# Kernel tuning notes

Hardware: AMD Instinct MI355X
Metric: run time of the kernel (lower is better)

Reference implementation:

```python
import jax, jax.numpy as jnp
import numpy as np

B, S, D_MODEL, H, D = 2, 2048, 1024, 16, 64
SCALE = 1.0 / float(np.sqrt(D))


def setup_inputs() -> dict:
    key = jax.random.key(0)
    ks = jax.random.split(key, 5)
    x = jax.random.normal(ks[0], (B, S, D_MODEL), jnp.float32)
    qkv_w = jax.random.normal(ks[1], (3 * H * D, D_MODEL), jnp.float32) * 0.02
    out_w = jax.random.normal(ks[2], (D_MODEL, H * D), jnp.float32) * 0.02
    bias_p = jax.random.uniform(ks[3], (H, 1, 1), jnp.float32) * 2.0  # torch.rand(...)*2
    bias_a = jax.random.uniform(ks[4], (H, 1, 1), jnp.float32)
    # standard geometric RoPE frequencies over d_head//2 = 32 channels
    rope_freqs = 10000.0 ** (-jnp.arange(D // 2, dtype=jnp.float32) / (D // 2))
    return {"x": x, "qkv_w": qkv_w, "out_w": out_w,
            "bias_p": bias_p, "bias_a": bias_a, "rope_freqs": rope_freqs}


def _rope(t, c, s):
    # t: [B,H,S,d]; c,s: [1,1,S,d/2]. Split-half rotation as in apply_rope.
    d2 = t.shape[-1] // 2
    t1, t2 = t[..., :d2], t[..., d2:]
    return jnp.concatenate([t1 * c - t2 * s, t1 * s + t2 * c], axis=-1)


def reference(x, qkv_w, out_w, bias_p, bias_a, rope_freqs):
    Bb, Ss, _ = x.shape
    qkv = (x @ qkv_w.T).reshape(Bb, Ss, 3, H, D)
    q = qkv[:, :, 0].transpose(0, 2, 1, 3)  # [B,H,S,d]
    k = qkv[:, :, 1].transpose(0, 2, 1, 3)
    v = qkv[:, :, 2].transpose(0, 2, 1, 3)
    pos = jnp.arange(Ss, dtype=jnp.float32)
    ang = pos[:, None] * rope_freqs[None, :]                 # [S, d/2]
    c = jnp.cos(ang)[None, None]
    s = jnp.sin(ang)[None, None]
    q = _rope(q, c, s)
    k = _rope(k, c, s)
    scores = jnp.einsum('bhqd,bhkd->bhqk', q, k) * SCALE     # [B,H,S,S]
    p = jnp.maximum(bias_p, 0.01)                            # clamp(min=0.01)
    a = jnp.maximum(bias_a, 0.01)
    dist = jnp.abs(pos[None, :] - pos[:, None])              # [S,S]
    kb = -p * jnp.log1p(a * dist)                            # [H,S,S]
    attn = jax.nn.softmax(scores + kb[None], axis=-1)
    out = jnp.einsum('bhqk,bhkd->bhqd', attn, v)             # [B,H,S,d]
    out = out.transpose(0, 2, 1, 3).reshape(Bb, Ss, H * D)
    return out @ out_w.T
```

## Files before the change

### kernel.cpp

```cpp
#include <hip/hip_runtime.h>
#include <math.h>

#define BATCH  2
#define SEQ    2048
#define DMODEL 1024
#define NH     16
#define HD     64
#define NQKV   3072
#define ROWS   (BATCH*SEQ)
#define QSCALE 0.18033688f

typedef unsigned short u16;
typedef unsigned int   u32;
typedef __bf16 bf16x8 __attribute__((ext_vector_type(8)));
typedef float  f32x4  __attribute__((ext_vector_type(4)));

typedef const __attribute__((address_space(1))) void* gptr_t;
typedef __attribute__((address_space(3))) void* lptr_t;

__device__ __forceinline__ void gload16(lptr_t l, const void* g) {
    __builtin_amdgcn_global_load_lds((gptr_t)g, l, 16, 0, 0);
}

__device__ __forceinline__ u16 f2bf(float f) {
    unsigned int u = __float_as_uint(f);
    u += 0x7FFFu + ((u >> 16) & 1u);
    return (u16)(u >> 16);
}
__device__ __forceinline__ u32 pk2(float lo, float hi) {
#if __has_builtin(__builtin_amdgcn_cvt_pk_bf16_f32)
    typedef __bf16 bf16x2 __attribute__((ext_vector_type(2)));
    union { bf16x2 v; u32 u; } cv;
    cv.v = __builtin_amdgcn_cvt_pk_bf16_f32(lo, hi);
    return cv.u;
#else
    return (u32)f2bf(lo) | ((u32)f2bf(hi) << 16);
#endif
}
__device__ __forceinline__ float fexp2(float x) {
#if __has_builtin(__builtin_amdgcn_exp2f)
    return __builtin_amdgcn_exp2f(x);
#else
    return exp2f(x);
#endif
}

#define NBC ((ROWS*DMODEL + NQKV*DMODEL + DMODEL*DMODEL) / 1024)
__global__ void prep_kernel(const float* __restrict__ a,
                            const float* __restrict__ b,
                            const float* __restrict__ c,
                            u16* __restrict__ oa, u16* __restrict__ ob,
                            u16* __restrict__ oc,
                            const float* __restrict__ freqs, float* __restrict__ cs_tab,
                            const float* __restrict__ bias_p,
                            const float* __restrict__ bias_a,
                            float* __restrict__ wtab)
{
    const int na = ROWS*DMODEL, nb = NQKV*DMODEL;
    int blk = blockIdx.x;
    if (blk < NBC) {
        int i = (blk * 256 + threadIdx.x) * 4;
        const float* s; u16* d; int base;
        if (i < na)           { s = a; d = oa; base = i; }
        else if (i < na + nb) { s = b; d = ob; base = i - na; }
        else                  { s = c; d = oc; base = i - na - nb; }
        float4 v = *(const float4*)(s + base);
        u16 o[4] = { f2bf(v.x), f2bf(v.y), f2bf(v.z), f2bf(v.w) };
        *(uint2*)(d + base) = *(const uint2*)o;
    } else if (blk < NBC + 256) {
        int idx = (blk - NBC) * 256 + threadIdx.x;
        int s = idx >> 5, d = idx & 31;
        float sn, cs;
        sincosf((float)s * freqs[d], &sn, &cs);
        cs_tab[idx * 2]     = cs;
        cs_tab[idx * 2 + 1] = sn;
    } else {
        int idx = (blk - NBC - 256) * 256 + threadIdx.x;
        int h = idx >> 11;
        int d = idx & (SEQ - 1);
        float p = fmaxf(bias_p[h], 0.01f);
        float aa = fmaxf(bias_a[h], 0.01f);
        wtab[idx] = __expf(-p * log1pf(aa * (float)d));
    }
}

__global__ __launch_bounds__(256) void gemm_qkv(
    const u16* __restrict__ A, const u16* __restrict__ B,
    const float* __restrict__ cs_tab,
    u16* __restrict__ Qb, u16* __restrict__ Kb, u16* __restrict__ Vt)
{
    const int K = DMODEL;
    __shared__ __align__(16) u16 As[128][32];
    __shared__ __align__(16) u16 Bs[128][32];
    const int tid  = threadIdx.x;
    const int wave = tid >> 6, lane = tid & 63;
    const int quad = lane >> 4, l16 = lane & 15;
    const int wrow = (wave >> 1) * 64, wcol = (wave & 1) * 64;
    const int bm = blockIdx.x * 128, bn = blockIdx.y * 128;

    const int srow = lane >> 2;
    const int scol = ((lane & 3) ^ (srow & 3)) * 8;
    const int fsw = (quad ^ (l16 & 3)) * 8;

    f32x4 acc[4][4];
#pragma unroll
    for (int i = 0; i < 4; ++i)
#pragma unroll
        for (int j = 0; j < 4; ++j) acc[i][j] = (f32x4){0.f,0.f,0.f,0.f};

    const u16* Ag0 = A + (size_t)(bm + wave*32 + srow)      * K + scol;
    const u16* Ag1 = A + (size_t)(bm + wave*32 + 16 + srow) * K + scol;
    const u16* Bg0 = B + (size_t)(bn + wave*32 + srow)      * K + scol;
    const u16* Bg1 = B + (size_t)(bn + wave*32 + 16 + srow) * K + scol;

    for (int k0 = 0; k0 < K; k0 += 32) {
        __syncthreads();
        gload16((lptr_t)&As[wave*32][0],      Ag0 + k0);
        gload16((lptr_t)&As[wave*32 + 16][0], Ag1 + k0);
        gload16((lptr_t)&Bs[wave*32][0],      Bg0 + k0);
        gload16((lptr_t)&Bs[wave*32 + 16][0], Bg1 + k0);
        __syncthreads();
        bf16x8 af[4], bfr[4];
#pragma unroll
        for (int i = 0; i < 4; ++i)
            af[i] = *(const bf16x8*)&As[wrow + i*16 + l16][fsw];
#pragma unroll
        for (int j = 0; j < 4; ++j)
            bfr[j] = *(const bf16x8*)&Bs[wcol + j*16 + l16][fsw];
#pragma unroll
        for (int i = 0; i < 4; ++i)
#pragma unroll
            for (int j = 0; j < 4; ++j)
                acc[i][j] = __builtin_amdgcn_mfma_f32_16x16x32_bf16(af[i], bfr[j], acc[i][j], 0, 0, 0);
    }

    const int tcol = (bn + wcol) >> 6;
    const int t = tcol >> 4, h = tcol & 15;
    const int bq = bm >> 11;
    const int sb = (bm & (SEQ - 1)) + wrow;
    const size_t hb = (size_t)(bq * NH + h) * SEQ * HD;

    if (t == 2) {
#pragma unroll
        for (int i = 0; i < 4; ++i) {
            const int s = sb + i*16 + quad*4;
#pragma unroll
            for (int j = 0; j < 4; ++j) {
                const int d = j*16 + l16;
                uint2 pv = make_uint2(pk2(acc[i][j][0], acc[i][j][1]),
                                      pk2(acc[i][j][2], acc[i][j][3]));
                *(uint2*)&Vt[hb + (size_t)d * SEQ + s] = pv;
            }
        }
    } else {
        const float sc = (t == 0) ? QSCALE : 1.0f;
        u16* dstb = ((t == 0) ? Qb : Kb) + hb;
#pragma unroll
        for (int i = 0; i < 4; ++i) {
#pragma unroll
            for (int r = 0; r < 4; ++r) {
                const int s = sb + i*16 + quad*4 + r;
                const float2* ct = (const float2*)(cs_tab + ((size_t)s * 32 + l16) * 2);
                float2 cs0 = ct[0];
                float2 cs1 = ct[16];
                float a0 = acc[i][0][r], a1 = acc[i][1][r];
                float a2 = acc[i][2][r], a3 = acc[i][3][r];
                u16* dst = dstb + (size_t)s * HD;
                dst[l16]      = f2bf((a0*cs0.x - a2*cs0.y) * sc);
                dst[16 + l16] = f2bf((a1*cs1.x - a3*cs1.y) * sc);
                dst[32 + l16] = f2bf((a0*cs0.y + a2*cs0.x) * sc);
                dst[48 + l16] = f2bf((a1*cs1.y + a3*cs1.x) * sc);
            }
        }
    }
}

__global__ __launch_bounds__(256) void gemm_out(
    const u16* __restrict__ A, const u16* __restrict__ B,
    float* __restrict__ Cout, int M, int N, int K)
{
    __shared__ __align__(16) u16 As[128][32];
    __shared__ __align__(16) u16 Bs[64][32];
    const int tid  = threadIdx.x;
    const int wave = tid >> 6, lane = tid & 63;
    const int quad = lane >> 4, l16 = lane & 15;
    const int wrow = (wave >> 1) * 64, wcol = (wave & 1) * 32;
    const int bm = blockIdx.x * 128, bn = blockIdx.y * 64;

    const int srow = lane >> 2;
    const int scol = ((lane & 3) ^ (srow & 3)) * 8;
    const int fsw = (quad ^ (l16 & 3)) * 8;

    f32x4 acc[4][2];
#pragma unroll
    for (int i = 0; i < 4; ++i)
#pragma unroll
        for (int j = 0; j < 2; ++j) acc[i][j] = (f32x4){0.f,0.f,0.f,0.f};

    const u16* Ag0 = A + (size_t)(bm + wave*32 + srow)      * K + scol;
    const u16* Ag1 = A + (size_t)(bm + wave*32 + 16 + srow) * K + scol;
    const u16* Bg0 = B + (size_t)(bn + wave*16 + srow)      * K + scol;

    for (int k0 = 0; k0 < K; k0 += 32) {
        __syncthreads();
        gload16((lptr_t)&As[wave*32][0],      Ag0 + k0);
        gload16((lptr_t)&As[wave*32 + 16][0], Ag1 + k0);
        gload16((lptr_t)&Bs[wave*16][0],      Bg0 + k0);
        __syncthreads();
        bf16x8 af[4], bfr[2];
#pragma unroll
        for (int i = 0; i < 4; ++i)
            af[i] = *(const bf16x8*)&As[wrow + i*16 + l16][fsw];
#pragma unroll
        for (int j = 0; j < 2; ++j)
            bfr[j] = *(const bf16x8*)&Bs[wcol + j*16 + l16][fsw];
#pragma unroll
        for (int i = 0; i < 4; ++i)
#pragma unroll
            for (int j = 0; j < 2; ++j)
                acc[i][j] = __builtin_amdgcn_mfma_f32_16x16x32_bf16(af[i], bfr[j], acc[i][j], 0, 0, 0);
    }

#pragma unroll
    for (int i = 0; i < 4; ++i)
#pragma unroll
        for (int j = 0; j < 2; ++j) {
            int col = bn + wcol + j*16 + l16;
#pragma unroll
            for (int r = 0; r < 4; ++r) {
                int row = bm + wrow + i*16 + quad*4 + r;
                Cout[(size_t)row * N + col] = acc[i][j][r];
            }
        }
}

__global__ __launch_bounds__(256, 3) void attn_mfma(
    const u16* __restrict__ Qb, const u16* __restrict__ Kb,
    const u16* __restrict__ Vt, const float* __restrict__ wtab,
    u16* __restrict__ attn_bf)
{
    __shared__ __align__(16) u16 Vs[2][64*128];
    __shared__ __align__(16) u16 Ps[4*64*32];
    __shared__ u32 ws2[2][192];
    __shared__ float lred[4][64];
    __shared__ float linv[64];

    const int tid = threadIdx.x;
    const int wave = tid >> 6, lane = tid & 63;
    const int quad = lane >> 4, l16 = lane & 15;
    const int q0 = blockIdx.x * 64, h = blockIdx.y, b = blockIdx.z;

    const u16* Qh = Qb + (size_t)(b * NH + h) * SEQ * HD;
    const u16* Kh = Kb + (size_t)(b * NH + h) * SEQ * HD;
    const u16* Vh = Vt + (size_t)(b * NH + h) * HD * SEQ;
    const float* wh = wtab + h * SEQ;

    bf16x8 qf0[4], qf1[4];
#pragma unroll
    for (int qj = 0; qj < 4; ++qj) {
        const u16* qr = Qh + (size_t)(q0 + qj*16 + l16) * HD + quad * 8;
        qf0[qj] = *(const bf16x8*)qr;
        qf1[qj] = *(const bf16x8*)(qr + 32);
    }

    const u16* Kf0 = Kh + (size_t)(wave*32 + l16) * HD + quad * 8;

    const int vsrow = lane >> 4;
    const u16* Vst[4];
#pragma unroll
    for (int i = 0; i < 4; ++i) {
        int d = wave*16 + i*4 + vsrow;
        int vscol = ((lane & 15) ^ (d & 7)) * 8;
        Vst[i] = Vh + (size_t)d * SEQ + vscol;
    }

    const int psw  = ((l16 >> 1) & 3) << 3;
    const int mb0  = 127 + l16 - wave*32 - quad*4 - 3;

    float l_p[4] = {0.f, 0.f, 0.f, 0.f};
    f32x4 o[4];
#pragma unroll
    for (int j = 0; j < 4; ++j) o[j] = (f32x4){0.f,0.f,0.f,0.f};

#pragma unroll
    for (int i = 0; i < 4; ++i)
        gload16((lptr_t)&Vs[0][(wave*16 + i*4)*128], Vst[i]);
    if (tid < 192) {
        int i0 = (q0 - 127) + tid;
        int a0 = i0 < 0 ? -i0 : i0;  if (a0 > SEQ-1) a0 = SEQ-1;
        int i1 = i0 + 1;
        int a1 = i1 < 0 ? -i1 : i1;  if (a1 > SEQ-1) a1 = SEQ-1;
        ws2[0][tid] = pk2(wh[a0], wh[a1]);
    }
    __syncthreads();

    for (int kt = 0; kt < SEQ / 128; ++kt) {
        const int k0 = kt * 128;
        const int cur = kt & 1;
        const u32* wsb = ws2[cur];

        bf16x8 kf[2][2];
#pragma unroll
        for (int kg = 0; kg < 2; ++kg) {
            const u16* kp = Kf0 + (size_t)(k0 + kg*16) * HD;
            kf[kg][0] = *(const bf16x8*)kp;
            kf[kg][1] = *(const bf16x8*)(kp + 32);
        }

        if (kt + 1 < SEQ / 128) {
#pragma unroll
            for (int i = 0; i < 4; ++i)
                gload16((lptr_t)&Vs[cur ^ 1][(wave*16 + i*4)*128],
                        Vst[i] + k0 + 128);
        }

#pragma unroll
        for (int kg = 0; kg < 2; ++kg) {
#pragma unroll
            for (int qj = 0; qj < 4; ++qj) {
                f32x4 zz = (f32x4){0.f,0.f,0.f,0.f};
                zz = __builtin_amdgcn_mfma_f32_16x16x32_bf16(kf[kg][0], qf0[qj], zz, 0, 0, 0);
                zz = __builtin_amdgcn_mfma_f32_16x16x32_bf16(kf[kg][1], qf1[qj], zz, 0, 0, 0);
                const int mbase = mb0 + qj*16 - kg*16;
                u32 pA = wsb[mbase], pB = wsb[mbase + 2];
                float w3 = __uint_as_float(pA << 16);
                float w2 = __uint_as_float(pA & 0xffff0000u);
                float w1 = __uint_as_float(pB << 16);
                float w0 = __uint_as_float(pB & 0xffff0000u);
                float e0 = fexp2(zz[0]) * w0, e1 = fexp2(zz[1]) * w1;
                float e2 = fexp2(zz[2]) * w2, e3 = fexp2(zz[3]) * w3;
                l_p[qj] += (e0 + e1) + (e2 + e3);
                *(uint2*)&Ps[wave*2048 + (qj*16 + l16)*32
                             + ((kg*16 + quad*4) ^ psw)] =
                    make_uint2(pk2(e0, e1), pk2(e2, e3));
            }
        }
        __syncthreads();

        bf16x8 pf[4];
#pragma unroll
        for (int m = 0; m < 4; ++m)
            pf[m] = *(const bf16x8*)&Ps[m*2048 + (wave*16 + l16)*32
                                        + ((quad*8) ^ psw)];
#pragma unroll
        for (int j = 0; j < 4; ++j) {
            const int vrow = (j*16 + l16) * 128;
            const int vsw = l16 & 7;
#pragma unroll
            for (int m = 0; m < 4; ++m) {
                bf16x8 vf = *(const bf16x8*)&Vs[cur][vrow + (((m*4 + quad) ^ vsw) * 8)];
                o[j] = __builtin_amdgcn_mfma_f32_16x16x32_bf16(pf[m], vf, o[j], 0, 0, 0);
            }
        }

        if (kt + 1 < SEQ / 128 && tid < 192) {
            int i0 = (q0 - (k0 + 128) - 127) + tid;
            int a0 = i0 < 0 ? -i0 : i0;  if (a0 > SEQ-1) a0 = SEQ-1;
            int i1 = i0 + 1;
            int a1 = i1 < 0 ? -i1 : i1;  if (a1 > SEQ-1) a1 = SEQ-1;
            ws2[cur ^ 1][tid] = pk2(wh[a0], wh[a1]);
        }
        __syncthreads();
    }

#pragma unroll
    for (int qj = 0; qj < 4; ++qj) {
        float l = l_p[qj];
        l += __shfl_xor(l, 16);
        l += __shfl_xor(l, 32);
        if (quad == 0) lred[wave][qj*16 + l16] = l;
    }
    __syncthreads();
    if (tid < 64)
        linv[tid] = 1.0f / (lred[0][tid] + lred[1][tid] + lred[2][tid] + lred[3][tid]);
    __syncthreads();
#pragma unroll
    for (int r = 0; r < 4; ++r) {
        const int q = wave*16 + quad*4 + r;
        float inv = linv[q];
        u16* dst = attn_bf + (size_t)(b * SEQ + q0 + q) * DMODEL + h * HD;
#pragma unroll
        for (int j = 0; j < 4; ++j)
            dst[j*16 + l16] = f2bf(o[j][r] * inv);
    }
}

extern "C" void kernel_launch(void* const* d_in, const int* in_sizes, int n_in,
                              void* d_out, int out_size, void* d_ws, size_t ws_size,
                              hipStream_t stream)
{
    (void)in_sizes; (void)n_in; (void)out_size; (void)ws_size;
    const float* x      = (const float*)d_in[0];
    const float* qkv_w  = (const float*)d_in[1];
    const float* out_w  = (const float*)d_in[2];
    const float* bias_p = (const float*)d_in[3];
    const float* bias_a = (const float*)d_in[4];
    const float* freqs  = (const float*)d_in[5];
    float* out = (float*)d_out;

    char* ws = (char*)d_ws;
    u16*   attn_bf = (u16*)ws;
    u16*   Qb      = (u16*)(ws + 8388608);
    u16*   x_bf    = (u16*)(ws + 25165824);
    u16*   w1_bf   = (u16*)(ws + 33554432);
    u16*   w2_bf   = (u16*)(ws + 39845888);
    u16*   Kb      = (u16*)(ws + 41943040);
    u16*   Vt      = (u16*)(ws + 50331648);
    float* wtab    = (float*)(ws + 58720256);
    float* cs_tab  = (float*)(ws + 58720256 + 131072);

    prep_kernel<<<dim3(NBC + 256 + 128), 256, 0, stream>>>(
        x, qkv_w, out_w, x_bf, w1_bf, w2_bf, freqs, cs_tab, bias_p, bias_a, wtab);

    gemm_qkv<<<dim3(ROWS/128, NQKV/128), 256, 0, stream>>>(x_bf, w1_bf, cs_tab, Qb, Kb, Vt);
    attn_mfma<<<dim3(SEQ/64, NH, BATCH), 256, 0, stream>>>(Qb, Kb, Vt, wtab, attn_bf);
    gemm_out<<<dim3(ROWS/128, DMODEL/64), 256, 0, stream>>>(attn_bf, w2_bf, out, ROWS, DMODEL, DMODEL);
}
```

Measured before the change: 239.4 us.

## Keep P in registers by giving each wave its own query rows

The attention kernel changes its work split. Each wave now owns 16 query rows and computes scores against all 128 keys of a tile, instead of owning a slice of keys across all 64 queries. The exponentiated probabilities stay in registers and feed the PV MFMA directly, which removes the Ps shared-memory round trip, a per-tile __syncthreads, and the cross-wave row-sum reduction. V fragments are now assembled from two 8-byte LDS reads to match the register layout of P, K loads are split into two halves around a sched_barrier, and launch bounds rise to 4 blocks per CU; each wave now reads every K row of a tile itself, so per-block K traffic grows.

```diff
diff --git a/kernel.cpp b/kernel.cpp
--- a/kernel.cpp
+++ b/kernel.cpp
@@ -8,6 +8,7 @@
 #define HD     64
 #define NQKV   3072
 #define ROWS   (BATCH*SEQ)
+#define NT     (SEQ/128)
 #define QSCALE 0.18033688f
 
 typedef unsigned short u16;
@@ -234,15 +235,13 @@
         }
 }
 
-__global__ __launch_bounds__(256, 3) void attn_mfma(
+__global__ __launch_bounds__(256, 4) void attn_mfma(
     const u16* __restrict__ Qb, const u16* __restrict__ Kb,
     const u16* __restrict__ Vt, const float* __restrict__ wtab,
     u16* __restrict__ attn_bf)
 {
     __shared__ __align__(16) u16 Vs[2][64*128];
-    __shared__ __align__(16) u16 Ps[4*64*32];
     __shared__ u32 ws2[2][192];
-    __shared__ float lred[4][64];
     __shared__ float linv[64];
 
     const int tid = threadIdx.x;
@@ -255,15 +254,11 @@
     const u16* Vh = Vt + (size_t)(b * NH + h) * HD * SEQ;
     const float* wh = wtab + h * SEQ;
 
-    bf16x8 qf0[4], qf1[4];
-#pragma unroll
-    for (int qj = 0; qj < 4; ++qj) {
-        const u16* qr = Qh + (size_t)(q0 + qj*16 + l16) * HD + quad * 8;
-        qf0[qj] = *(const bf16x8*)qr;
-        qf1[qj] = *(const bf16x8*)(qr + 32);
-    }
-
-    const u16* Kf0 = Kh + (size_t)(wave*32 + l16) * HD + quad * 8;
+    const u16* qr = Qh + (size_t)(q0 + wave*16 + l16) * HD + quad * 8;
+    const bf16x8 qf0 = *(const bf16x8*)qr;
+    const bf16x8 qf1 = *(const bf16x8*)(qr + 32);
+
+    const u16* Kf = Kh + (size_t)l16 * HD + quad * 8;
 
     const int vsrow = lane >> 4;
     const u16* Vst[4];
@@ -274,10 +269,9 @@
         Vst[i] = Vh + (size_t)d * SEQ + vscol;
     }
 
-    const int psw  = ((l16 >> 1) & 3) << 3;
-    const int mb0  = 127 + l16 - wave*32 - quad*4 - 3;
-
-    float l_p[4] = {0.f, 0.f, 0.f, 0.f};
+    const int mb0 = 127 + wave*16 + l16 - quad*4 - 3;
+
+    float l_p = 0.f;
     f32x4 o[4];
 #pragma unroll
     for (int j = 0; j < 4; ++j) o[j] = (f32x4){0.f,0.f,0.f,0.f};
@@ -294,67 +288,91 @@
     }
     __syncthreads();
 
-    for (int kt = 0; kt < SEQ / 128; ++kt) {
-        const int k0 = kt * 128;
+    for (int kt = 0; kt < NT; ++kt) {
         const int cur = kt & 1;
         const u32* wsb = ws2[cur];
-
-        bf16x8 kf[2][2];
-#pragma unroll
-        for (int kg = 0; kg < 2; ++kg) {
-            const u16* kp = Kf0 + (size_t)(k0 + kg*16) * HD;
-            kf[kg][0] = *(const bf16x8*)kp;
-            kf[kg][1] = *(const bf16x8*)(kp + 32);
-        }
-
-        if (kt + 1 < SEQ / 128) {
+        const u16* Kt = Kf + (size_t)(kt * 128) * HD;
+        u32 y[16];
+        bf16x8 ka[8];
+
+#pragma unroll
+        for (int g = 0; g < 4; ++g) {
+            const u16* kp = Kt + (size_t)(g * 16) * HD;
+            ka[2*g]   = *(const bf16x8*)kp;
+            ka[2*g+1] = *(const bf16x8*)(kp + 32);
+        }
+#pragma unroll
+        for (int g = 0; g < 4; ++g) {
+            f32x4 z = (f32x4){0.f,0.f,0.f,0.f};
+            z = __builtin_amdgcn_mfma_f32_16x16x32_bf16(ka[2*g],   qf0, z, 0, 0, 0);
+            z = __builtin_amdgcn_mfma_f32_16x16x32_bf16(ka[2*g+1], qf1, z, 0, 0, 0);
+            const int mbase = mb0 - 16*g;
+            u32 pA = wsb[mbase], pB = wsb[mbase + 2];
+            float w3 = __uint_as_float(pA << 16);
+            float w2 = __uint_as_float(pA & 0xffff0000u);
+            float w1 = __uint_as_float(pB << 16);
+            float w0 = __uint_as_float(pB & 0xffff0000u);
+            float e0 = fexp2(z[0]) * w0, e1 = fexp2(z[1]) * w1;
+            float e2 = fexp2(z[2]) * w2, e3 = fexp2(z[3]) * w3;
+            l_p += (e0 + e1) + (e2 + e3);
+            y[2*g]   = pk2(e0, e1);
+            y[2*g+1] = pk2(e2, e3);
+        }
+
+#pragma unroll
+        for (int g = 0; g < 4; ++g) {
+            const u16* kp = Kt + (size_t)((g + 4) * 16) * HD;
+            ka[2*g]   = *(const bf16x8*)kp;
+            ka[2*g+1] = *(const bf16x8*)(kp + 32);
+        }
+        __builtin_amdgcn_sched_barrier(0);
+
+        if (kt + 1 < NT) {
 #pragma unroll
             for (int i = 0; i < 4; ++i)
                 gload16((lptr_t)&Vs[cur ^ 1][(wave*16 + i*4)*128],
-                        Vst[i] + k0 + 128);
-        }
-
-#pragma unroll
-        for (int kg = 0; kg < 2; ++kg) {
-#pragma unroll
-            for (int qj = 0; qj < 4; ++qj) {
-                f32x4 zz = (f32x4){0.f,0.f,0.f,0.f};
-                zz = __builtin_amdgcn_mfma_f32_16x16x32_bf16(kf[kg][0], qf0[qj], zz, 0, 0, 0);
-                zz = __builtin_amdgcn_mfma_f32_16x16x32_bf16(kf[kg][1], qf1[qj], zz, 0, 0, 0);
-                const int mbase = mb0 + qj*16 - kg*16;
-                u32 pA = wsb[mbase], pB = wsb[mbase + 2];
-                float w3 = __uint_as_float(pA << 16);
-                float w2 = __uint_as_float(pA & 0xffff0000u);
-                float w1 = __uint_as_float(pB << 16);
-                float w0 = __uint_as_float(pB & 0xffff0000u);
-                float e0 = fexp2(zz[0]) * w0, e1 = fexp2(zz[1]) * w1;
-                float e2 = fexp2(zz[2]) * w2, e3 = fexp2(zz[3]) * w3;
-                l_p[qj] += (e0 + e1) + (e2 + e3);
-                *(uint2*)&Ps[wave*2048 + (qj*16 + l16)*32
-                             + ((kg*16 + quad*4) ^ psw)] =
-                    make_uint2(pk2(e0, e1), pk2(e2, e3));
+                        Vst[i] + (kt + 1) * 128);
+        }
+
+#pragma unroll
+        for (int g = 0; g < 4; ++g) {
+            f32x4 z = (f32x4){0.f,0.f,0.f,0.f};
+            z = __builtin_amdgcn_mfma_f32_16x16x32_bf16(ka[2*g],   qf0, z, 0, 0, 0);
+            z = __builtin_amdgcn_mfma_f32_16x16x32_bf16(ka[2*g+1], qf1, z, 0, 0, 0);
+            const int mbase = mb0 - 16*(g + 4);
+            u32 pA = wsb[mbase], pB = wsb[mbase + 2];
+            float w3 = __uint_as_float(pA << 16);
+            float w2 = __uint_as_float(pA & 0xffff0000u);
+            float w1 = __uint_as_float(pB << 16);
+            float w0 = __uint_as_float(pB & 0xffff0000u);
+            float e0 = fexp2(z[0]) * w0, e1 = fexp2(z[1]) * w1;
+            float e2 = fexp2(z[2]) * w2, e3 = fexp2(z[3]) * w3;
+            l_p += (e0 + e1) + (e2 + e3);
+            y[8 + 2*g] = pk2(e0, e1);
+            y[9 + 2*g] = pk2(e2, e3);
+        }
+
+#pragma unroll
+        for (int s = 0; s < 4; ++s) {
+            union { u32 u[4]; bf16x8 v; } pfu;
+            pfu.u[0] = y[4*s];     pfu.u[1] = y[4*s + 1];
+            pfu.u[2] = y[4*s + 2]; pfu.u[3] = y[4*s + 3];
+#pragma unroll
+            for (int j = 0; j < 4; ++j) {
+                const int d = j*16 + l16;
+                const int rb = d*128 + (quad & 1)*4;
+                const int c0 = (4*s     + (quad >> 1)) ^ (l16 & 7);
+                const int c1 = (4*s + 2 + (quad >> 1)) ^ (l16 & 7);
+                uint2 va = *(const uint2*)&Vs[cur][rb + c0*8];
+                uint2 vb = *(const uint2*)&Vs[cur][rb + c1*8];
+                union { uint4 u; bf16x8 v; } vfu;
+                vfu.u = make_uint4(va.x, va.y, vb.x, vb.y);
+                o[j] = __builtin_amdgcn_mfma_f32_16x16x32_bf16(pfu.v, vfu.v, o[j], 0, 0, 0);
             }
         }
-        __syncthreads();
-
-        bf16x8 pf[4];
-#pragma unroll
-        for (int m = 0; m < 4; ++m)
-            pf[m] = *(const bf16x8*)&Ps[m*2048 + (wave*16 + l16)*32
-                                        + ((quad*8) ^ psw)];
-#pragma unroll
-        for (int j = 0; j < 4; ++j) {
-            const int vrow = (j*16 + l16) * 128;
-            const int vsw = l16 & 7;
-#pragma unroll
-            for (int m = 0; m < 4; ++m) {
-                bf16x8 vf = *(const bf16x8*)&Vs[cur][vrow + (((m*4 + quad) ^ vsw) * 8)];
-                o[j] = __builtin_amdgcn_mfma_f32_16x16x32_bf16(pf[m], vf, o[j], 0, 0, 0);
-            }
-        }
-
-        if (kt + 1 < SEQ / 128 && tid < 192) {
-            int i0 = (q0 - (k0 + 128) - 127) + tid;
+
+        if (kt + 1 < NT && tid < 192) {
+            int i0 = (q0 - (kt + 1)*128 - 127) + tid;
             int a0 = i0 < 0 ? -i0 : i0;  if (a0 > SEQ-1) a0 = SEQ-1;
             int i1 = i0 + 1;
             int a1 = i1 < 0 ? -i1 : i1;  if (a1 > SEQ-1) a1 = SEQ-1;
@@ -363,16 +381,9 @@
         __syncthreads();
     }
 
-#pragma unroll
-    for (int qj = 0; qj < 4; ++qj) {
-        float l = l_p[qj];
-        l += __shfl_xor(l, 16);
-        l += __shfl_xor(l, 32);
-        if (quad == 0) lred[wave][qj*16 + l16] = l;
-    }
-    __syncthreads();
-    if (tid < 64)
-        linv[tid] = 1.0f / (lred[0][tid] + lred[1][tid] + lred[2][tid] + lred[3][tid]);
+    l_p += __shfl_xor(l_p, 16);
+    l_p += __shfl_xor(l_p, 32);
+    if (quad == 0) linv[wave*16 + l16] = 1.0f / l_p;
     __syncthreads();
 #pragma unroll
     for (int r = 0; r < 4; ++r) {
```

After: 285.5 us. 19.3% more time.

## Keep softmax probabilities in registers by splitting waves over query and key halves

Applied to the files above, without the earlier changes.

The attention kernel's wave work split changes from one key slice per wave across all queries to a 2x2 split over query halves and key halves. Each wave's probability tile can then feed the PV MFMA directly from registers. This removes the Ps shared-memory buffer and the mid-iteration __syncthreads that went with it. In exchange, the two key-half partial outputs must be combined through shared memory at the end, each wave holds more accumulator registers, and V fragments are gathered with narrower 8-byte LDS reads.

```diff
diff --git a/kernel.cpp b/kernel.cpp
--- a/kernel.cpp
+++ b/kernel.cpp
@@ -8,6 +8,7 @@
 #define HD     64
 #define NQKV   3072
 #define ROWS   (BATCH*SEQ)
+#define NT     (SEQ/128)
 #define QSCALE 0.18033688f
 
 typedef unsigned short u16;
@@ -240,14 +241,14 @@
     u16* __restrict__ attn_bf)
 {
     __shared__ __align__(16) u16 Vs[2][64*128];
-    __shared__ __align__(16) u16 Ps[4*64*32];
     __shared__ u32 ws2[2][192];
-    __shared__ float lred[4][64];
+    __shared__ float lred[4][32];
     __shared__ float linv[64];
 
     const int tid = threadIdx.x;
     const int wave = tid >> 6, lane = tid & 63;
     const int quad = lane >> 4, l16 = lane & 15;
+    const int qh = wave >> 1, kh = wave & 1;
     const int q0 = blockIdx.x * 64, h = blockIdx.y, b = blockIdx.z;
 
     const u16* Qh = Qb + (size_t)(b * NH + h) * SEQ * HD;
@@ -255,15 +256,15 @@
     const u16* Vh = Vt + (size_t)(b * NH + h) * HD * SEQ;
     const float* wh = wtab + h * SEQ;
 
-    bf16x8 qf0[4], qf1[4];
-#pragma unroll
-    for (int qj = 0; qj < 4; ++qj) {
-        const u16* qr = Qh + (size_t)(q0 + qj*16 + l16) * HD + quad * 8;
+    bf16x8 qf0[2], qf1[2];
+#pragma unroll
+    for (int qj = 0; qj < 2; ++qj) {
+        const u16* qr = Qh + (size_t)(q0 + qh*32 + qj*16 + l16) * HD + quad * 8;
         qf0[qj] = *(const bf16x8*)qr;
         qf1[qj] = *(const bf16x8*)(qr + 32);
     }
 
-    const u16* Kf0 = Kh + (size_t)(wave*32 + l16) * HD + quad * 8;
+    const u16* Kf = Kh + (size_t)(kh*64 + l16) * HD + quad * 8;
 
     const int vsrow = lane >> 4;
     const u16* Vst[4];
@@ -274,13 +275,14 @@
         Vst[i] = Vh + (size_t)d * SEQ + vscol;
     }
 
-    const int psw  = ((l16 >> 1) & 3) << 3;
-    const int mb0  = 127 + l16 - wave*32 - quad*4 - 3;
-
-    float l_p[4] = {0.f, 0.f, 0.f, 0.f};
-    f32x4 o[4];
-#pragma unroll
-    for (int j = 0; j < 4; ++j) o[j] = (f32x4){0.f,0.f,0.f,0.f};
+    const int mb0 = 127 + qh*32 + l16 - kh*64 - quad*4 - 3;
+
+    float l_p[2] = {0.f, 0.f};
+    f32x4 o[2][4];
+#pragma unroll
+    for (int qj = 0; qj < 2; ++qj)
+#pragma unroll
+        for (int dj = 0; dj < 4; ++dj) o[qj][dj] = (f32x4){0.f,0.f,0.f,0.f};
 
 #pragma unroll
     for (int i = 0; i < 4; ++i)
@@ -294,67 +296,75 @@
     }
     __syncthreads();
 
-    for (int kt = 0; kt < SEQ / 128; ++kt) {
-        const int k0 = kt * 128;
+    for (int kt = 0; kt < NT; ++kt) {
         const int cur = kt & 1;
         const u32* wsb = ws2[cur];
-
-        bf16x8 kf[2][2];
-#pragma unroll
-        for (int kg = 0; kg < 2; ++kg) {
-            const u16* kp = Kf0 + (size_t)(k0 + kg*16) * HD;
-            kf[kg][0] = *(const bf16x8*)kp;
-            kf[kg][1] = *(const bf16x8*)(kp + 32);
-        }
-
-        if (kt + 1 < SEQ / 128) {
+        const u16* Kt = Kf + (size_t)(kt * 128) * HD;
+
+        bf16x8 kf[4][2];
+#pragma unroll
+        for (int g = 0; g < 4; ++g) {
+            const u16* kp = Kt + (size_t)(g * 16) * HD;
+            kf[g][0] = *(const bf16x8*)kp;
+            kf[g][1] = *(const bf16x8*)(kp + 32);
+        }
+        __builtin_amdgcn_sched_barrier(0);
+
+        if (kt + 1 < NT) {
 #pragma unroll
             for (int i = 0; i < 4; ++i)
                 gload16((lptr_t)&Vs[cur ^ 1][(wave*16 + i*4)*128],
-                        Vst[i] + k0 + 128);
-        }
-
-#pragma unroll
-        for (int kg = 0; kg < 2; ++kg) {
-#pragma unroll
-            for (int qj = 0; qj < 4; ++qj) {
-                f32x4 zz = (f32x4){0.f,0.f,0.f,0.f};
-                zz = __builtin_amdgcn_mfma_f32_16x16x32_bf16(kf[kg][0], qf0[qj], zz, 0, 0, 0);
-                zz = __builtin_amdgcn_mfma_f32_16x16x32_bf16(kf[kg][1], qf1[qj], zz, 0, 0, 0);
-                const int mbase = mb0 + qj*16 - kg*16;
+                        Vst[i] + (kt + 1) * 128);
+        }
+
+        u32 y[2][8];
+#pragma unroll
+        for (int g = 0; g < 4; ++g) {
+#pragma unroll
+            for (int qj = 0; qj < 2; ++qj) {
+                f32x4 z = (f32x4){0.f,0.f,0.f,0.f};
+                z = __builtin_amdgcn_mfma_f32_16x16x32_bf16(kf[g][0], qf0[qj], z, 0, 0, 0);
+                z = __builtin_amdgcn_mfma_f32_16x16x32_bf16(kf[g][1], qf1[qj], z, 0, 0, 0);
+                const int mbase = mb0 + qj*16 - g*16;
                 u32 pA = wsb[mbase], pB = wsb[mbase + 2];
                 float w3 = __uint_as_float(pA << 16);
                 float w2 = __uint_as_float(pA & 0xffff0000u);
                 float w1 = __uint_as_float(pB << 16);
                 float w0 = __uint_as_float(pB & 0xffff0000u);
-                float e0 = fexp2(zz[0]) * w0, e1 = fexp2(zz[1]) * w1;
-                float e2 = fexp2(zz[2]) * w2, e3 = fexp2(zz[3]) * w3;
+                float e0 = fexp2(z[0]) * w0, e1 = fexp2(z[1]) * w1;
+                float e2 = fexp2(z[2]) * w2, e3 = fexp2(z[3]) * w3;
                 l_p[qj] += (e0 + e1) + (e2 + e3);
-                *(uint2*)&Ps[wave*2048 + (qj*16 + l16)*32
-                             + ((kg*16 + quad*4) ^ psw)] =
-                    make_uint2(pk2(e0, e1), pk2(e2, e3));
-            }
-        }
-        __syncthreads();
-
-        bf16x8 pf[4];
-#pragma unroll
-        for (int m = 0; m < 4; ++m)
-            pf[m] = *(const bf16x8*)&Ps[m*2048 + (wave*16 + l16)*32
-                                        + ((quad*8) ^ psw)];
-#pragma unroll
-        for (int j = 0; j < 4; ++j) {
-            const int vrow = (j*16 + l16) * 128;
-            const int vsw = l16 & 7;
-#pragma unroll
-            for (int m = 0; m < 4; ++m) {
-                bf16x8 vf = *(const bf16x8*)&Vs[cur][vrow + (((m*4 + quad) ^ vsw) * 8)];
-                o[j] = __builtin_amdgcn_mfma_f32_16x16x32_bf16(pf[m], vf, o[j], 0, 0, 0);
-            }
-        }
-
-        if (kt + 1 < SEQ / 128 && tid < 192) {
-            int i0 = (q0 - (k0 + 128) - 127) + tid;
+                y[qj][g*2]     = pk2(e0, e1);
+                y[qj][g*2 + 1] = pk2(e2, e3);
+            }
+        }
+
+#pragma unroll
+        for (int dj = 0; dj < 4; ++dj) {
+            const int drow = (dj*16 + l16) * 128;
+            const int cbase = kh*8 + (quad >> 1);
+            const int coff  = (quad & 1) * 4;
+            uint2 v00 = *(const uint2*)&Vs[cur][drow + (((cbase    ) ^ (l16 & 7)) * 8) + coff];
+            uint2 v01 = *(const uint2*)&Vs[cur][drow + (((cbase + 2) ^ (l16 & 7)) * 8) + coff];
+            uint2 v10 = *(const uint2*)&Vs[cur][drow + (((cbase + 4) ^ (l16 & 7)) * 8) + coff];
+            uint2 v11 = *(const uint2*)&Vs[cur][drow + (((cbase + 6) ^ (l16 & 7)) * 8) + coff];
+            union { uint4 u; bf16x8 v; } vf0, vf1;
+            vf0.u = make_uint4(v00.x, v00.y, v01.x, v01.y);
+            vf1.u = make_uint4(v10.x, v10.y, v11.x, v11.y);
+#pragma unroll
+            for (int qj = 0; qj < 2; ++qj) {
+                union { u32 u[4]; bf16x8 v; } pf0, pf1;
+                pf0.u[0] = y[qj][0]; pf0.u[1] = y[qj][1];
+                pf0.u[2] = y[qj][2]; pf0.u[3] = y[qj][3];
+                pf1.u[0] = y[qj][4]; pf1.u[1] = y[qj][5];
+                pf1.u[2] = y[qj][6]; pf1.u[3] = y[qj][7];
+                o[qj][dj] = __builtin_amdgcn_mfma_f32_16x16x32_bf16(pf0.v, vf0.v, o[qj][dj], 0, 0, 0);
+                o[qj][dj] = __builtin_amdgcn_mfma_f32_16x16x32_bf16(pf1.v, vf1.v, o[qj][dj], 0, 0, 0);
+            }
+        }
+
+        if (kt + 1 < NT && tid < 192) {
+            int i0 = (q0 - (kt + 1)*128 - 127) + tid;
             int a0 = i0 < 0 ? -i0 : i0;  if (a0 > SEQ-1) a0 = SEQ-1;
             int i1 = i0 + 1;
             int a1 = i1 < 0 ? -i1 : i1;  if (a1 > SEQ-1) a1 = SEQ-1;
@@ -364,24 +374,39 @@
     }
 
 #pragma unroll
-    for (int qj = 0; qj < 4; ++qj) {
+    for (int qj = 0; qj < 2; ++qj) {
         float l = l_p[qj];
         l += __shfl_xor(l, 16);
         l += __shfl_xor(l, 32);
         if (quad == 0) lred[wave][qj*16 + l16] = l;
     }
+    float* sc = (float*)&Vs[0][0];
+    if (kh == 0) {
+#pragma unroll
+        for (int qj = 0; qj < 2; ++qj)
+#pragma unroll
+            for (int dj = 0; dj < 4; ++dj)
+#pragma unroll
+                for (int r = 0; r < 4; ++r)
+                    sc[(qh*32 + qj*16 + quad*4 + r)*68 + dj*16 + l16] = o[qj][dj][r];
+    }
     __syncthreads();
     if (tid < 64)
-        linv[tid] = 1.0f / (lred[0][tid] + lred[1][tid] + lred[2][tid] + lred[3][tid]);
+        linv[tid] = 1.0f / (lred[(tid >> 5)*2][tid & 31] + lred[(tid >> 5)*2 + 1][tid & 31]);
     __syncthreads();
-#pragma unroll
-    for (int r = 0; r < 4; ++r) {
-        const int q = wave*16 + quad*4 + r;
-        float inv = linv[q];
-        u16* dst = attn_bf + (size_t)(b * SEQ + q0 + q) * DMODEL + h * HD;
-#pragma unroll
-        for (int j = 0; j < 4; ++j)
-            dst[j*16 + l16] = f2bf(o[j][r] * inv);
+    if (kh == 1) {
+#pragma unroll
+        for (int qj = 0; qj < 2; ++qj)
+#pragma unroll
+            for (int r = 0; r < 4; ++r) {
+                const int q = qh*32 + qj*16 + quad*4 + r;
+                float inv = linv[q];
+                u16* dst = attn_bf + (size_t)(b * SEQ + q0 + q) * DMODEL + h * HD;
+#pragma unroll
+                for (int dj = 0; dj < 4; ++dj)
+                    dst[dj*16 + l16] =
+                        f2bf((o[qj][dj][r] + sc[q*68 + dj*16 + l16]) * inv);
+            }
     }
 }
 
```

New measurement: 251.0 us. 4.8% more time.
